# Kernel tuning notes

Measured on AMD Instinct MI355X. Metric: run time of the kernel, lower is better.

## Reference

```python
import jax, jax.numpy as jnp
import numpy as np
import math

B, S, E = 4, 2048, 1024


def setup_inputs() -> dict:
    key = jax.random.key(0)
    ks = jax.random.split(key, 9)
    x = jax.random.normal(ks[0], (B, S, E), dtype=jnp.float32)
    # causal boolean mask, broadcast over batch: True = keep
    mask = jnp.broadcast_to(jnp.tril(jnp.ones((S, S), dtype=bool)), (B, S, S))
    sc = 1.0 / math.sqrt(E)
    Wq = jax.random.normal(ks[1], (E, E), dtype=jnp.float32) * sc
    bq = jnp.zeros((E,), dtype=jnp.float32)
    Wk = jax.random.normal(ks[2], (E, E), dtype=jnp.float32) * sc
    bk = jnp.zeros((E,), dtype=jnp.float32)
    Wv = jax.random.normal(ks[3], (E, E), dtype=jnp.float32) * sc
    bv = jnp.zeros((E,), dtype=jnp.float32)
    gamma = jnp.ones((E,), dtype=jnp.float32)
    beta = jnp.zeros((E,), dtype=jnp.float32)
    return {"x": x, "mask": mask, "Wq": Wq, "bq": bq, "Wk": Wk, "bk": bk,
            "Wv": Wv, "bv": bv, "gamma": gamma, "beta": beta}


def reference(x, mask, Wq, bq, Wk, bk, Wv, bv, gamma, beta):
    E_ = x.shape[-1]
    q = jnp.einsum('bse,fe->bsf', x, Wq) + bq
    k = jnp.einsum('bse,fe->bsf', x, Wk) + bk
    v = jnp.einsum('bse,fe->bsf', x, Wv) + bv
    scores = jnp.einsum('bqe,bke->bqk', q, k) / jnp.sqrt(jnp.float32(E_))
    scores = jnp.where(mask, scores, -jnp.inf)
    probs = jax.nn.softmax(scores, axis=-1)
    attn = jnp.einsum('bqk,bke->bqe', probs, v)
    y = attn + x
    # LayerNorm over last dim, eps matches torch default 1e-5
    mu = jnp.mean(y, axis=-1, keepdims=True)
    var = jnp.mean(jnp.square(y - mu), axis=-1, keepdims=True)
    return (y - mu) / jnp.sqrt(var + 1e-5) * gamma + beta
```

## Files before the change

kernel.cpp:

```cpp
#include <hip/hip_runtime.h>
#include <hip/hip_bf16.h>
#include <stdint.h>

#define B_ 4
#define S_ 2048
#define E_ 1024
#define BS_ (B_*S_)

using bf16x8 = __attribute__((ext_vector_type(8))) __bf16;
using f32x4  = __attribute__((ext_vector_type(4))) float;

__device__ __forceinline__ unsigned short f2bf(float f) {
  unsigned int u = __float_as_uint(f);
  u += 0x7fffu + ((u >> 16) & 1u);
  return (unsigned short)(u >> 16);
}
__device__ __forceinline__ float bf2f(unsigned short h) {
  return __uint_as_float(((unsigned int)h) << 16);
}

__device__ __forceinline__ void gld16(const unsigned short* g, unsigned short* l) {
  __builtin_amdgcn_global_load_lds((__attribute__((address_space(1))) void*)(void*)g,
                                   (__attribute__((address_space(3))) void*)l, 16, 0, 0);
}

__global__ __launch_bounds__(256) void conv_f32_bf16(const float* __restrict__ in,
                                                     unsigned short* __restrict__ out,
                                                     int n4) {
  int i = blockIdx.x * 256 + threadIdx.x;
  if (i >= n4) return;
  const float4 v = ((const float4*)in)[i];
  ushort4 o;
  o.x = f2bf(v.x); o.y = f2bf(v.y); o.z = f2bf(v.z); o.w = f2bf(v.w);
  ((ushort4*)out)[i] = o;
}

__global__ __launch_bounds__(256) void prep_w(
    const float* __restrict__ Wq, const float* __restrict__ Wk, const float* __restrict__ Wv,
    const float* __restrict__ bq, const float* __restrict__ bk, const float* __restrict__ bv,
    unsigned short* __restrict__ Wb, float* __restrict__ bb) {
  const int i = blockIdx.x * 256 + threadIdx.x;
  const int n4 = E_ * E_ / 4;
  if (i < 3 * n4) {
    const int m = i / n4, j = i - m * n4;
    const float* src = (m == 0) ? Wq : (m == 1) ? Wk : Wv;
    const float4 v = ((const float4*)src)[j];
    ushort4 o;
    o.x = f2bf(v.x); o.y = f2bf(v.y); o.z = f2bf(v.z); o.w = f2bf(v.w);
    ((ushort4*)Wb)[i] = o;
  } else {
    const int j = i - 3 * n4;
    if (j < 3 * E_) bb[j] = (j < E_) ? bq[j] : (j < 2 * E_) ? bk[j - E_] : bv[j - 2 * E_];
  }
}

template<int EPI>
__global__ __launch_bounds__(256, 3) void gemm_bt(
    const unsigned short* __restrict__ A, const unsigned short* __restrict__ Bm,
    float* __restrict__ Cf, unsigned short* __restrict__ Cb,
    const float* __restrict__ bias,
    int K, int lda, int ldb, int ldc,
    long sA, long sB, long sC, float scale, int causal)
{
  constexpr int BM = 128, BN = 128, BK = 64;
  __shared__ __align__(16) unsigned short As[BM * BK];
  __shared__ __align__(16) unsigned short Bs[BN * BK];
  const int bz = blockIdx.z;
  A  += sA * bz;
  Bm += sB * bz;
  const int mt = (EPI != 0) ? (gridDim.y - 1 - blockIdx.y) : blockIdx.y;
  const int m0 = mt * BM, n0 = blockIdx.x * BN;
  if (EPI == 1 && causal && n0 >= m0 + BM) return;
  const int kend = (EPI == 2 && causal) ? min(K, m0 + BM) : K;
  const int t = threadIdx.x;
  const int lane = t & 63, wave = t >> 6;
  const int wr = wave >> 1, wc = wave & 1;
  const int q = lane >> 4, r = lane & 15;

  const int srow   = lane >> 3;
  const int schunk = (lane & 7) ^ srow;
  const long ga0 = (long)(m0 + wave * 32 + srow) * lda + schunk * 8;
  const long gb0 = (long)(n0 + wave * 32 + srow) * ldb + schunk * 8;

  f32x4 acc[4][4] = {};

  for (int k0 = 0; k0 < kend; k0 += BK) {
#pragma unroll
    for (int s = 0; s < 4; ++s) {
      gld16(A  + ga0 + (long)s * 8 * lda + k0, &As[(wave * 32 + s * 8) * 64]);
      gld16(Bm + gb0 + (long)s * 8 * ldb + k0, &Bs[(wave * 32 + s * 8) * 64]);
    }
    __syncthreads();
#pragma unroll
    for (int kk = 0; kk < BK; kk += 32) {
      bf16x8 af[4], bfr[4];
      const int cq = (kk >> 3) + q;
#pragma unroll
      for (int i = 0; i < 4; ++i) {
        const int row = wr * 64 + i * 16 + r;
        af[i] = *(const bf16x8*)&As[(row * 8 + (cq ^ (r & 7))) * 8];
      }
#pragma unroll
      for (int j = 0; j < 4; ++j) {
        const int row = wc * 64 + j * 16 + r;
        bfr[j] = *(const bf16x8*)&Bs[(row * 8 + (cq ^ (r & 7))) * 8];
      }
#pragma unroll
      for (int i = 0; i < 4; ++i)
#pragma unroll
        for (int j = 0; j < 4; ++j)
          acc[i][j] = __builtin_amdgcn_mfma_f32_16x16x32_bf16(af[i], bfr[j], acc[i][j], 0, 0, 0);
    }
    __syncthreads();
  }

  if (EPI == 2) Cf += sC * bz; else Cb += sC * bz;
#pragma unroll
  for (int i = 0; i < 4; ++i) {
#pragma unroll
    for (int j = 0; j < 4; ++j) {
      const int col = n0 + wc * 64 + j * 16 + r;
#pragma unroll
      for (int e = 0; e < 4; ++e) {
        const int rowg = m0 + wr * 64 + i * 16 + q * 4 + e;
        float v = acc[i][j][e];
        if (EPI == 0) {
          v += bias[col];
          Cb[(long)rowg * ldc + col] = f2bf(v);
        } else if (EPI == 1) {
          Cb[(long)rowg * ldc + col] = f2bf(v * scale);
        } else {
          Cf[(long)rowg * ldc + col] = v;
        }
      }
    }
  }
}

__global__ __launch_bounds__(256) void transpose_b(const unsigned short* __restrict__ V,
                                                   unsigned short* __restrict__ Vt, int lda) {
  __shared__ unsigned short tile[64][68];
  const int b = blockIdx.z;
  const unsigned short* Vb = V + (long)b * S_ * lda;
  unsigned short* Vtb = Vt + (long)b * S_ * E_;
  const int e0 = blockIdx.x * 64, j0 = blockIdx.y * 64;
  const int t = threadIdx.x;
#pragma unroll
  for (int i = 0; i < 4; ++i) {
    const int c = t + i * 256;
    const int row = c >> 4, c4 = c & 15;
    *(ushort4*)&tile[row][c4 * 4] = *(const ushort4*)&Vb[(long)(j0 + row) * lda + e0 + c4 * 4];
  }
  __syncthreads();
#pragma unroll
  for (int i = 0; i < 4; ++i) {
    const int c = t + i * 256;
    const int orow = c >> 4, c4 = c & 15;
    ushort4 o;
    o.x = tile[c4 * 4 + 0][orow];
    o.y = tile[c4 * 4 + 1][orow];
    o.z = tile[c4 * 4 + 2][orow];
    o.w = tile[c4 * 4 + 3][orow];
    *(ushort4*)&Vtb[(long)(e0 + orow) * S_ + j0 + c4 * 4] = o;
  }
}

__global__ __launch_bounds__(256) void softmax_causal(unsigned short* __restrict__ Sc) {
  const int row = blockIdx.x * 4 + (threadIdx.x >> 6);
  const int lane = threadIdx.x & 63;
  const int b = row >> 11, ii = row & (S_ - 1);
  unsigned short* prow = Sc + (long)b * S_ * S_ + (long)ii * S_;
  const int len = ii + 1;
  float v[32];
#pragma unroll
  for (int c = 0; c < 4; ++c) {
    const int base = (c * 64 + lane) * 8;
    if (base < len) {
      const uint4 u = *(const uint4*)&prow[base];
      const unsigned int w[4] = {u.x, u.y, u.z, u.w};
#pragma unroll
      for (int e = 0; e < 8; ++e) {
        const unsigned short h = (unsigned short)(w[e >> 1] >> ((e & 1) * 16));
        v[c * 8 + e] = (base + e < len) ? bf2f(h) : -3.0e38f;
      }
    } else {
#pragma unroll
      for (int e = 0; e < 8; ++e) v[c * 8 + e] = -3.0e38f;
    }
  }
  float mx = -3.0e38f;
#pragma unroll
  for (int i = 0; i < 32; ++i) mx = fmaxf(mx, v[i]);
#pragma unroll
  for (int o = 32; o; o >>= 1) mx = fmaxf(mx, __shfl_xor(mx, o));
  float sum = 0.f;
#pragma unroll
  for (int i = 0; i < 32; ++i) { v[i] = __expf(v[i] - mx); sum += v[i]; }
#pragma unroll
  for (int o = 32; o; o >>= 1) sum += __shfl_xor(sum, o);
  const float inv = 1.0f / sum;
#pragma unroll
  for (int c = 0; c < 4; ++c) {
    const int base = (c * 64 + lane) * 8;
    uint4 u;
    unsigned int w[4];
#pragma unroll
    for (int p = 0; p < 4; ++p) {
      const unsigned short lo = f2bf(v[c * 8 + p * 2] * inv);
      const unsigned short hi = f2bf(v[c * 8 + p * 2 + 1] * inv);
      w[p] = (unsigned int)lo | ((unsigned int)hi << 16);
    }
    u.x = w[0]; u.y = w[1]; u.z = w[2]; u.w = w[3];
    *(uint4*)&prow[base] = u;
  }
}

__global__ __launch_bounds__(256) void residual_ln(
    const float* __restrict__ attn, const float* __restrict__ x,
    const float* __restrict__ gamma, const float* __restrict__ beta,
    float* __restrict__ out) {
  __shared__ float rs[4], rs2[4];
  const long row = blockIdx.x;
  const int t = threadIdx.x;
  const int lane = t & 63, wave = t >> 6;
  const float4 a  = ((const float4*)(attn + row * E_))[t];
  const float4 xv = ((const float4*)(x + row * E_))[t];
  const float y0 = a.x + xv.x, y1 = a.y + xv.y, y2 = a.z + xv.z, y3 = a.w + xv.w;
  float s  = y0 + y1 + y2 + y3;
  float s2 = y0 * y0 + y1 * y1 + y2 * y2 + y3 * y3;
#pragma unroll
  for (int o = 32; o; o >>= 1) { s += __shfl_xor(s, o); s2 += __shfl_xor(s2, o); }
  if (lane == 0) { rs[wave] = s; rs2[wave] = s2; }
  __syncthreads();
  s  = rs[0] + rs[1] + rs[2] + rs[3];
  s2 = rs2[0] + rs2[1] + rs2[2] + rs2[3];
  const float mu  = s * (1.0f / E_);
  const float var = s2 * (1.0f / E_) - mu * mu;
  const float inv = rsqrtf(var + 1e-5f);
  const float4 g  = ((const float4*)gamma)[t];
  const float4 be = ((const float4*)beta)[t];
  float4 o;
  o.x = (y0 - mu) * inv * g.x + be.x;
  o.y = (y1 - mu) * inv * g.y + be.y;
  o.z = (y2 - mu) * inv * g.z + be.z;
  o.w = (y3 - mu) * inv * g.w + be.w;
  ((float4*)(out + row * E_))[t] = o;
}

extern "C" void kernel_launch(void* const* d_in, const int* in_sizes, int n_in,
                              void* d_out, int out_size, void* d_ws, size_t ws_size,
                              hipStream_t stream) {
  const float* x  = (const float*)d_in[0];
  const float* Wq = (const float*)d_in[2];
  const float* bq = (const float*)d_in[3];
  const float* Wk = (const float*)d_in[4];
  const float* bk = (const float*)d_in[5];
  const float* Wv = (const float*)d_in[6];
  const float* bv = (const float*)d_in[7];
  const float* gamma = (const float*)d_in[8];
  const float* beta  = (const float*)d_in[9];
  float* out = (float*)d_out;

  char* ws = (char*)d_ws;
  size_t off = 0;
  auto alloc = [&](size_t bytes) { char* p = ws + off; off += (bytes + 255) & ~(size_t)255; return p; };
  unsigned short* xb    = (unsigned short*)alloc((size_t)BS_ * E_ * 2);
  unsigned short* Wqkvb = (unsigned short*)alloc((size_t)3 * E_ * E_ * 2);
  float*          bqkv  = (float*)alloc((size_t)3 * E_ * 4);
  unsigned short* Cqkv  = (unsigned short*)alloc((size_t)BS_ * 3 * E_ * 2);
  unsigned short* Vt    = (unsigned short*)alloc((size_t)BS_ * E_ * 2);
  unsigned short* Sc    = (unsigned short*)alloc((size_t)B_ * S_ * S_ * 2);
  float* attn = (float*)Cqkv;

  conv_f32_bf16<<<dim3(BS_ * E_ / 4 / 256), 256, 0, stream>>>(x, xb, BS_ * E_ / 4);
  prep_w<<<dim3((3 * E_ * E_ / 4 + 3 * E_ + 255) / 256), 256, 0, stream>>>(
      Wq, Wk, Wv, bq, bk, bv, Wqkvb, bqkv);

  dim3 g1(3 * E_ / 128, BS_ / 128, 1);
  gemm_bt<0><<<g1, 256, 0, stream>>>(xb, Wqkvb, nullptr, Cqkv, bqkv,
                                     E_, E_, E_, 3 * E_, 0, 0, 0, 1.f, 0);

  transpose_b<<<dim3(E_ / 64, S_ / 64, B_), 256, 0, stream>>>(Cqkv + 2 * E_, Vt, 3 * E_);

  dim3 g2(S_ / 128, S_ / 128, B_);
  gemm_bt<1><<<g2, 256, 0, stream>>>(Cqkv, Cqkv + E_, nullptr, Sc, nullptr,
                                     E_, 3 * E_, 3 * E_, S_,
                                     (long)S_ * 3 * E_, (long)S_ * 3 * E_, (long)S_ * S_,
                                     0.03125f, 1);

  softmax_causal<<<dim3(BS_ / 4), 256, 0, stream>>>(Sc);

  dim3 g3(E_ / 128, S_ / 128, B_);
  gemm_bt<2><<<g3, 256, 0, stream>>>(Sc, Vt, attn, nullptr, nullptr,
                                     S_, S_, S_, E_,
                                     (long)S_ * S_, (long)S_ * E_, (long)S_ * E_, 1.f, 1);

  residual_ln<<<dim3(BS_), 256, 0, stream>>>(attn, x, gamma, beta, out);
}
```

Baseline: 307.3 us.

## Fuse V transpose into QKV GEMM, triangular QK grid, split-K PV for balance

The QKV GEMM epilogue now writes V directly in transposed layout, which removes the separate transpose kernel and shrinks the Cqkv buffer. The QK^T GEMM launches only the lower-triangular tiles through a linear-to-triangular index map, so no blocks exit early. The PV GEMM splits the long-K row tiles into two halves written to separate buffers, and residual_ln sums them, which evens out per-block work across the causal triangle. The softmax skips writing tiles above the diagonal block, and the x and weight conversions are merged into one prep kernel. The cost is an extra fp32 partial buffer plus an extra read in the layernorm, and uncoalesced 8-byte strided stores for Vt.

```diff
diff --git a/kernel.cpp b/kernel.cpp
--- a/kernel.cpp
+++ b/kernel.cpp
@@ -10,6 +10,9 @@
 using bf16x8 = __attribute__((ext_vector_type(8))) __bf16;
 using f32x4  = __attribute__((ext_vector_type(4))) float;
 
+__constant__ int pv_mt[24] = {7,8,9,10,11,12,13,14,15,15,14,6,13,5,12,4,11,3,10,2,9,1,8,0};
+__constant__ int pv_ck[24] = {0,0,0,0,0,0,0,0,0, 1, 1,0, 1,0, 1,0, 1,0, 1,0, 1,0, 1,0};
+
 __device__ __forceinline__ unsigned short f2bf(float f) {
   unsigned int u = __float_as_uint(f);
   u += 0x7fffu + ((u >> 16) & 1u);
@@ -24,32 +27,28 @@
                                    (__attribute__((address_space(3))) void*)l, 16, 0, 0);
 }
 
-__global__ __launch_bounds__(256) void conv_f32_bf16(const float* __restrict__ in,
-                                                     unsigned short* __restrict__ out,
-                                                     int n4) {
-  int i = blockIdx.x * 256 + threadIdx.x;
-  if (i >= n4) return;
-  const float4 v = ((const float4*)in)[i];
-  ushort4 o;
-  o.x = f2bf(v.x); o.y = f2bf(v.y); o.z = f2bf(v.z); o.w = f2bf(v.w);
-  ((ushort4*)out)[i] = o;
-}
-
-__global__ __launch_bounds__(256) void prep_w(
+__global__ __launch_bounds__(256) void prep_all(
+    const float* __restrict__ x,
     const float* __restrict__ Wq, const float* __restrict__ Wk, const float* __restrict__ Wv,
     const float* __restrict__ bq, const float* __restrict__ bk, const float* __restrict__ bv,
-    unsigned short* __restrict__ Wb, float* __restrict__ bb) {
+    unsigned short* __restrict__ xb, unsigned short* __restrict__ Wb, float* __restrict__ bb) {
   const int i = blockIdx.x * 256 + threadIdx.x;
-  const int n4 = E_ * E_ / 4;
-  if (i < 3 * n4) {
-    const int m = i / n4, j = i - m * n4;
-    const float* src = (m == 0) ? Wq : (m == 1) ? Wk : Wv;
-    const float4 v = ((const float4*)src)[j];
+  const int nx4 = BS_ * E_ / 4, nw4 = E_ * E_ / 4;
+  if (i < nx4) {
+    const float4 v = ((const float4*)x)[i];
     ushort4 o;
     o.x = f2bf(v.x); o.y = f2bf(v.y); o.z = f2bf(v.z); o.w = f2bf(v.w);
-    ((ushort4*)Wb)[i] = o;
+    ((ushort4*)xb)[i] = o;
+  } else if (i < nx4 + 3 * nw4) {
+    const int j = i - nx4;
+    const int m = j / nw4, jj = j - m * nw4;
+    const float* src = (m == 0) ? Wq : (m == 1) ? Wk : Wv;
+    const float4 v = ((const float4*)src)[jj];
+    ushort4 o;
+    o.x = f2bf(v.x); o.y = f2bf(v.y); o.z = f2bf(v.z); o.w = f2bf(v.w);
+    ((ushort4*)Wb)[j] = o;
   } else {
-    const int j = i - 3 * n4;
+    const int j = i - nx4 - 3 * nw4;
     if (j < 3 * E_) bb[j] = (j < E_) ? bq[j] : (j < 2 * E_) ? bk[j - E_] : bv[j - 2 * E_];
   }
 }
@@ -57,10 +56,11 @@
 template<int EPI>
 __global__ __launch_bounds__(256, 3) void gemm_bt(
     const unsigned short* __restrict__ A, const unsigned short* __restrict__ Bm,
-    float* __restrict__ Cf, unsigned short* __restrict__ Cb,
+    float* __restrict__ Cf, float* __restrict__ Cf2,
+    unsigned short* __restrict__ Cb, unsigned short* __restrict__ VtOut,
     const float* __restrict__ bias,
     int K, int lda, int ldb, int ldc,
-    long sA, long sB, long sC, float scale, int causal)
+    long sA, long sB, long sC, float scale)
 {
   constexpr int BM = 128, BN = 128, BK = 64;
   __shared__ __align__(16) unsigned short As[BM * BK];
@@ -68,10 +68,23 @@
   const int bz = blockIdx.z;
   A  += sA * bz;
   Bm += sB * bz;
-  const int mt = (EPI != 0) ? (gridDim.y - 1 - blockIdx.y) : blockIdx.y;
-  const int m0 = mt * BM, n0 = blockIdx.x * BN;
-  if (EPI == 1 && causal && n0 >= m0 + BM) return;
-  const int kend = (EPI == 2 && causal) ? min(K, m0 + BM) : K;
+
+  int mt, nt, ck = 0;
+  if (EPI == 1) {
+    const int id = blockIdx.x;
+    mt = (int)((sqrtf(8.f * id + 1.f) - 1.f) * 0.5f);
+    while ((mt * (mt + 1)) / 2 > id) --mt;
+    while (((mt + 1) * (mt + 2)) / 2 <= id) ++mt;
+    nt = id - (mt * (mt + 1)) / 2;
+  } else if (EPI == 2) {
+    mt = pv_mt[blockIdx.y]; ck = pv_ck[blockIdx.y]; nt = blockIdx.x;
+  } else {
+    mt = blockIdx.y; nt = blockIdx.x;
+  }
+  const int m0 = mt * BM, n0 = nt * BN;
+  const int k0s  = (EPI == 2 && ck) ? 1024 : 0;
+  const int kend = (EPI == 2) ? (ck ? m0 + BM : min(1024, m0 + BM)) : K;
+
   const int t = threadIdx.x;
   const int lane = t & 63, wave = t >> 6;
   const int wr = wave >> 1, wc = wave & 1;
@@ -84,7 +97,7 @@
 
   f32x4 acc[4][4] = {};
 
-  for (int k0 = 0; k0 < kend; k0 += BK) {
+  for (int k0 = k0s; k0 < kend; k0 += BK) {
 #pragma unroll
     for (int s = 0; s < 4; ++s) {
       gld16(A  + ga0 + (long)s * 8 * lda + k0, &As[(wave * 32 + s * 8) * 64]);
@@ -114,54 +127,65 @@
     __syncthreads();
   }
 
-  if (EPI == 2) Cf += sC * bz; else Cb += sC * bz;
-#pragma unroll
-  for (int i = 0; i < 4; ++i) {
-#pragma unroll
-    for (int j = 0; j < 4; ++j) {
-      const int col = n0 + wc * 64 + j * 16 + r;
-#pragma unroll
-      for (int e = 0; e < 4; ++e) {
-        const int rowg = m0 + wr * 64 + i * 16 + q * 4 + e;
-        float v = acc[i][j][e];
-        if (EPI == 0) {
-          v += bias[col];
-          Cb[(long)rowg * ldc + col] = f2bf(v);
-        } else if (EPI == 1) {
-          Cb[(long)rowg * ldc + col] = f2bf(v * scale);
-        } else {
-          Cf[(long)rowg * ldc + col] = v;
+  if (EPI == 0) {
+    if (n0 < 2 * E_) {
+#pragma unroll
+      for (int i = 0; i < 4; ++i)
+#pragma unroll
+        for (int j = 0; j < 4; ++j) {
+          const int col = n0 + wc * 64 + j * 16 + r;
+          const float bia = bias[col];
+#pragma unroll
+          for (int e = 0; e < 4; ++e) {
+            const int rowg = m0 + wr * 64 + i * 16 + q * 4 + e;
+            Cb[(long)rowg * ldc + col] = f2bf(acc[i][j][e] + bia);
+          }
         }
-      }
-    }
-  }
-}
-
-__global__ __launch_bounds__(256) void transpose_b(const unsigned short* __restrict__ V,
-                                                   unsigned short* __restrict__ Vt, int lda) {
-  __shared__ unsigned short tile[64][68];
-  const int b = blockIdx.z;
-  const unsigned short* Vb = V + (long)b * S_ * lda;
-  unsigned short* Vtb = Vt + (long)b * S_ * E_;
-  const int e0 = blockIdx.x * 64, j0 = blockIdx.y * 64;
-  const int t = threadIdx.x;
-#pragma unroll
-  for (int i = 0; i < 4; ++i) {
-    const int c = t + i * 256;
-    const int row = c >> 4, c4 = c & 15;
-    *(ushort4*)&tile[row][c4 * 4] = *(const ushort4*)&Vb[(long)(j0 + row) * lda + e0 + c4 * 4];
-  }
-  __syncthreads();
-#pragma unroll
-  for (int i = 0; i < 4; ++i) {
-    const int c = t + i * 256;
-    const int orow = c >> 4, c4 = c & 15;
-    ushort4 o;
-    o.x = tile[c4 * 4 + 0][orow];
-    o.y = tile[c4 * 4 + 1][orow];
-    o.z = tile[c4 * 4 + 2][orow];
-    o.w = tile[c4 * 4 + 3][orow];
-    *(ushort4*)&Vtb[(long)(e0 + orow) * S_ + j0 + c4 * 4] = o;
+    } else {
+#pragma unroll
+      for (int i = 0; i < 4; ++i) {
+        const int base = m0 + wr * 64 + i * 16 + q * 4;
+        const int b = base >> 11, s0 = base & (S_ - 1);
+#pragma unroll
+        for (int j = 0; j < 4; ++j) {
+          const int col = n0 + wc * 64 + j * 16 + r;
+          const int e_ = col - 2 * E_;
+          const float bia = bias[col];
+          ushort4 o;
+          o.x = f2bf(acc[i][j][0] + bia);
+          o.y = f2bf(acc[i][j][1] + bia);
+          o.z = f2bf(acc[i][j][2] + bia);
+          o.w = f2bf(acc[i][j][3] + bia);
+          *(ushort4*)&VtOut[((long)b * E_ + e_) * S_ + s0] = o;
+        }
+      }
+    }
+  } else if (EPI == 1) {
+    Cb += sC * bz;
+#pragma unroll
+    for (int i = 0; i < 4; ++i)
+#pragma unroll
+      for (int j = 0; j < 4; ++j) {
+        const int col = n0 + wc * 64 + j * 16 + r;
+#pragma unroll
+        for (int e = 0; e < 4; ++e) {
+          const int rowg = m0 + wr * 64 + i * 16 + q * 4 + e;
+          Cb[(long)rowg * ldc + col] = f2bf(acc[i][j][e] * scale);
+        }
+      }
+  } else {
+    float* dst = (ck ? Cf2 : Cf) + sC * bz;
+#pragma unroll
+    for (int i = 0; i < 4; ++i)
+#pragma unroll
+      for (int j = 0; j < 4; ++j) {
+        const int col = n0 + wc * 64 + j * 16 + r;
+#pragma unroll
+        for (int e = 0; e < 4; ++e) {
+          const int rowg = m0 + wr * 64 + i * 16 + q * 4 + e;
+          dst[(long)rowg * ldc + col] = acc[i][j][e];
+        }
+      }
   }
 }
 
@@ -171,6 +195,7 @@
   const int b = row >> 11, ii = row & (S_ - 1);
   unsigned short* prow = Sc + (long)b * S_ * S_ + (long)ii * S_;
   const int len = ii + 1;
+  const int wend = ((ii >> 7) + 1) << 7;
   float v[32];
 #pragma unroll
   for (int c = 0; c < 4; ++c) {
@@ -202,6 +227,7 @@
 #pragma unroll
   for (int c = 0; c < 4; ++c) {
     const int base = (c * 64 + lane) * 8;
+    if (base >= wend) continue;
     uint4 u;
     unsigned int w[4];
 #pragma unroll
@@ -216,7 +242,8 @@
 }
 
 __global__ __launch_bounds__(256) void residual_ln(
-    const float* __restrict__ attn, const float* __restrict__ x,
+    const float* __restrict__ attn, const float* __restrict__ attn2,
+    const float* __restrict__ x,
     const float* __restrict__ gamma, const float* __restrict__ beta,
     float* __restrict__ out) {
   __shared__ float rs[4], rs2[4];
@@ -225,7 +252,10 @@
   const int lane = t & 63, wave = t >> 6;
   const float4 a  = ((const float4*)(attn + row * E_))[t];
   const float4 xv = ((const float4*)(x + row * E_))[t];
-  const float y0 = a.x + xv.x, y1 = a.y + xv.y, y2 = a.z + xv.z, y3 = a.w + xv.w;
+  float4 a2 = make_float4(0.f, 0.f, 0.f, 0.f);
+  if ((row & (S_ - 1)) >= 1024) a2 = ((const float4*)(attn2 + row * E_))[t];
+  const float y0 = a.x + a2.x + xv.x, y1 = a.y + a2.y + xv.y;
+  const float y2 = a.z + a2.z + xv.z, y3 = a.w + a2.w + xv.w;
   float s  = y0 + y1 + y2 + y3;
   float s2 = y0 * y0 + y1 * y1 + y2 * y2 + y3 * y3;
 #pragma unroll
@@ -267,33 +297,30 @@
   unsigned short* xb    = (unsigned short*)alloc((size_t)BS_ * E_ * 2);
   unsigned short* Wqkvb = (unsigned short*)alloc((size_t)3 * E_ * E_ * 2);
   float*          bqkv  = (float*)alloc((size_t)3 * E_ * 4);
-  unsigned short* Cqkv  = (unsigned short*)alloc((size_t)BS_ * 3 * E_ * 2);
+  unsigned short* Cqkv  = (unsigned short*)alloc((size_t)BS_ * 2 * E_ * 2);
   unsigned short* Vt    = (unsigned short*)alloc((size_t)BS_ * E_ * 2);
   unsigned short* Sc    = (unsigned short*)alloc((size_t)B_ * S_ * S_ * 2);
+  float*          attn2 = (float*)alloc((size_t)BS_ * E_ * 4);
   float* attn = (float*)Cqkv;
 
-  conv_f32_bf16<<<dim3(BS_ * E_ / 4 / 256), 256, 0, stream>>>(x, xb, BS_ * E_ / 4);
-  prep_w<<<dim3((3 * E_ * E_ / 4 + 3 * E_ + 255) / 256), 256, 0, stream>>>(
-      Wq, Wk, Wv, bq, bk, bv, Wqkvb, bqkv);
+  const int nprep = BS_ * E_ / 4 + 3 * E_ * E_ / 4 + 3 * E_;
+  prep_all<<<dim3((nprep + 255) / 256), 256, 0, stream>>>(x, Wq, Wk, Wv, bq, bk, bv, xb, Wqkvb, bqkv);
 
   dim3 g1(3 * E_ / 128, BS_ / 128, 1);
-  gemm_bt<0><<<g1, 256, 0, stream>>>(xb, Wqkvb, nullptr, Cqkv, bqkv,
-                                     E_, E_, E_, 3 * E_, 0, 0, 0, 1.f, 0);
-
-  transpose_b<<<dim3(E_ / 64, S_ / 64, B_), 256, 0, stream>>>(Cqkv + 2 * E_, Vt, 3 * E_);
-
-  dim3 g2(S_ / 128, S_ / 128, B_);
-  gemm_bt<1><<<g2, 256, 0, stream>>>(Cqkv, Cqkv + E_, nullptr, Sc, nullptr,
-                                     E_, 3 * E_, 3 * E_, S_,
-                                     (long)S_ * 3 * E_, (long)S_ * 3 * E_, (long)S_ * S_,
-                                     0.03125f, 1);
+  gemm_bt<0><<<g1, 256, 0, stream>>>(xb, Wqkvb, nullptr, nullptr, Cqkv, Vt, bqkv,
+                                     E_, E_, E_, 2 * E_, 0, 0, 0, 1.f);
+
+  dim3 g2(136, 1, B_);
+  gemm_bt<1><<<g2, 256, 0, stream>>>(Cqkv, Cqkv + E_, nullptr, nullptr, Sc, nullptr, nullptr,
+                                     E_, 2 * E_, 2 * E_, S_,
+                                     (long)S_ * 2 * E_, (long)S_ * 2 * E_, (long)S_ * S_, 0.03125f);
 
   softmax_causal<<<dim3(BS_ / 4), 256, 0, stream>>>(Sc);
 
-  dim3 g3(E_ / 128, S_ / 128, B_);
-  gemm_bt<2><<<g3, 256, 0, stream>>>(Sc, Vt, attn, nullptr, nullptr,
+  dim3 g3(E_ / 128, 24, B_);
+  gemm_bt<2><<<g3, 256, 0, stream>>>(Sc, Vt, attn, attn2, nullptr, nullptr, nullptr,
                                      S_, S_, S_, E_,
-                                     (long)S_ * S_, (long)S_ * E_, (long)S_ * E_, 1.f, 1);
-
-  residual_ln<<<dim3(BS_), 256, 0, stream>>>(attn, x, gamma, beta, out);
-}
+                                     (long)S_ * S_, (long)S_ * E_, (long)S_ * E_, 1.f);
+
+  residual_ln<<<dim3(BS_), 256, 0, stream>>>(attn, attn2, x, gamma, beta, out);
+}
```

Result: faster. 296.0 us (-3.7%).
